# Kernel optimization log

Hardware: AMD Instinct MI355X
Metric: run time of the kernel (lower is better)

The kernel has to match this reference:

```python
import jax, jax.numpy as jnp
import numpy as np

NUM_NODES_G1 = 60000
NUM_NODES_G2 = 50000
NUM_REL = 16
NUM_BASES = 4
DIM = 128  # node_dim == hidden_dim == final_dim
L_COMMON = 100


def _concept_layer(x, edge_index):
    # Gather-based concept propagation: x_i <- x_i + mean_{j in N(i)} x_j
    src, dst = edge_index[0], edge_index[1]
    n = x.shape[0]
    agg = jax.ops.segment_sum(x[src], dst, num_segments=n)
    deg = jax.ops.segment_sum(jnp.ones((src.shape[0],), x.dtype), dst, num_segments=n)
    return x + agg / jnp.clip(deg, 1.0)[:, None]


def _rgcn_layer(x, edge_index, edge_type, basis, comp, root, bias):
    # Basis-decomposed RGCN: out_i = x_i @ root + bias + sum_r (1/|N_i^r|) sum_{j in N_i^r} x_j @ W_r,
    # W_r = sum_b comp[r,b] * basis[b]. Reorder: scatter comp-weighted x[src] per basis, then one GEMM per basis.
    src, dst = edge_index[0], edge_index[1]
    n = x.shape[0]
    e = src.shape[0]
    seg = dst * NUM_REL + edge_type  # per-(node, relation) bucket
    cnt = jax.ops.segment_sum(jnp.ones((e,), x.dtype), seg, num_segments=n * NUM_REL)
    norm = 1.0 / jnp.clip(cnt, 1.0)
    coef = comp[edge_type] * norm[seg][:, None]  # [E, B]
    xsrc = x[src]  # [E, D] -- dominant gather traffic
    out = x @ root + bias
    for b in range(NUM_BASES):  # small fixed loop over bases
        agg_b = jax.ops.segment_sum(xsrc * coef[:, b:b + 1], dst, num_segments=n)
        out = out + agg_b @ basis[b]
    return out


def setup_inputs() -> dict:
    key = jax.random.key(0)
    ks = jax.random.split(key, 16)
    e2, e1 = 800000, 800000
    return {
        "edge_index_g2": jax.random.randint(ks[0], (2, e2), 0, NUM_NODES_G2),
        "edge_type_g2": jax.random.randint(ks[1], (e2,), 0, NUM_REL),
        "edge_index_g1": jax.random.randint(ks[2], (2, e1), 0, NUM_NODES_G1),
        "left_common": jax.random.randint(ks[3], (L_COMMON,), 0, NUM_NODES_G1),
        "all_node_embedding": jax.random.normal(ks[4], (NUM_NODES_G1, DIM), jnp.float32),
        "basis1": jax.random.normal(ks[5], (NUM_BASES, DIM, DIM), jnp.float32) * 0.05,
        "comp1": jax.random.normal(ks[6], (NUM_REL, NUM_BASES), jnp.float32),
        "root1": jax.random.normal(ks[7], (DIM, DIM), jnp.float32) * 0.05,
        "bias1": jnp.zeros((DIM,), jnp.float32),
        "basis2": jax.random.normal(ks[8], (NUM_BASES, DIM, DIM), jnp.float32) * 0.05,
        "comp2": jax.random.normal(ks[9], (NUM_REL, NUM_BASES), jnp.float32),
        "root2": jax.random.normal(ks[10], (DIM, DIM), jnp.float32) * 0.05,
        "bias2": jnp.zeros((DIM,), jnp.float32),
        "weights": jax.random.uniform(ks[11], (DIM, 1), jnp.float32),
    }


def reference(edge_index_g2, edge_type_g2, edge_index_g1, left_common,
              all_node_embedding, basis1, comp1, root1, bias1,
              basis2, comp2, root2, bias2, weights):
    x_g1 = jax.nn.relu(_concept_layer(all_node_embedding, edge_index_g1))
    x = x_g1[:NUM_NODES_G2]
    x = _rgcn_layer(x, edge_index_g2, edge_type_g2, basis1, comp1, root1, bias1)
    x = jax.nn.relu(x)  # relu_use == 1
    x_g2 = _rgcn_layer(x, edge_index_g2, edge_type_g2, basis2, comp2, root2, bias2)
    ty = x_g1[left_common]  # [L, D]
    # mul_def outer elementwise product followed by matmul with weights collapses to one contraction:
    # logits[n,l] = sum_d x_g2[n,d] * ty[l,d] * w[d]
    logits = jnp.einsum('nd,ld,d->nl', x_g2, ty, weights[:, 0])
    return jax.nn.softmax(logits, axis=1)
```

## Files before the change

kernel.cpp:

```cpp
#include <hip/hip_runtime.h>
#include <hip/hip_bf16.h>
#include <math.h>

#define N1 60000
#define N2 50000
#define DIM 128
#define NREL 16
#define NB 4
#define LCOM 100
#define LPAD 112

typedef __attribute__((ext_vector_type(8))) short short8;
typedef __attribute__((ext_vector_type(4))) float f32x4;
typedef __attribute__((ext_vector_type(4))) _Float16 half4;
typedef __attribute__((ext_vector_type(8))) _Float16 half8;

__device__ __forceinline__ float bf2f(unsigned short u) {
    union { unsigned int i; float f; } c; c.i = ((unsigned int)u) << 16; return c.f;
}
__device__ __forceinline__ unsigned short f2bf(float f) {
    union { float f; unsigned int i; } c; c.f = f;
    unsigned int r = c.i + 0x7FFF + ((c.i >> 16) & 1);
    return (unsigned short)(r >> 16);
}
__device__ __forceinline__ void split8(float4 a, float4 b, short8& h, short8& l) {
    float f[8] = {a.x, a.y, a.z, a.w, b.x, b.y, b.z, b.w};
#pragma unroll
    for (int j = 0; j < 8; j++) {
        unsigned short hh = f2bf(f[j]);
        h[j] = (short)hh;
        l[j] = (short)f2bf(f[j] - bf2f(hh));
    }
}

__global__ __launch_bounds__(256) void k_prelude(
        const int* __restrict__ ei1, int E1, int* __restrict__ deg1, int HB1,
        const int* __restrict__ ei2, int E2, int* __restrict__ deg2, int HB2,
        const float* __restrict__ root1, const float* __restrict__ basis1,
        unsigned short* __restrict__ Wh1, unsigned short* __restrict__ Wl1,
        const float* __restrict__ root2, const float* __restrict__ basis2,
        unsigned short* __restrict__ Wh2, unsigned short* __restrict__ Wl2, int PB,
        const float* __restrict__ emb, _Float16* __restrict__ embh, int n4) {
    int b = blockIdx.x;
    if (b < HB1) {
        int e0 = b * 1024 + threadIdx.x;
#pragma unroll
        for (int j = 0; j < 4; j++) {
            int e = e0 + j * 256;
            if (e < E1) atomicAdd(deg1 + ei1[E1 + e], 1);
        }
    } else if (b < HB1 + HB2) {
        int e0 = (b - HB1) * 1024 + threadIdx.x;
#pragma unroll
        for (int j = 0; j < 4; j++) {
            int e = e0 + j * 256;
            if (e < E2) atomicAdd(deg2 + ei2[E2 + e], 1);
        }
    } else if (b < HB1 + HB2 + PB) {
        int t = (b - HB1 - HB2) * 256 + threadIdx.x;
        if (t < 2 * 640 * 128) {
            int which = t >= 640 * 128;
            int tt = which ? t - 640 * 128 : t;
            const float* root = which ? root2 : root1;
            const float* basis = which ? basis2 : basis1;
            unsigned short* Wh = which ? Wh2 : Wh1;
            unsigned short* Wl = which ? Wl2 : Wl1;
            int k = tt >> 7, n = tt & 127;
            float v = (k < 128) ? root[k * 128 + n] : basis[(k - 128) * 128 + n];
            unsigned short h = f2bf(v);
            Wh[n * 640 + k] = h;
            Wl[n * 640 + k] = f2bf(v - bf2f(h));
        }
    } else {
        int i = (b - HB1 - HB2 - PB) * 256 + threadIdx.x;
        if (i < n4) {
            float4 v = ((const float4*)emb)[i];
            half4 o = {(_Float16)v.x, (_Float16)v.y, (_Float16)v.z, (_Float16)v.w};
            ((half4*)embh)[i] = o;
        }
    }
}

__global__ __launch_bounds__(256) void k_scan_p1m(const int* __restrict__ inA, int nA, int nbA,
                                                  int* __restrict__ bsumA,
                                                  const int* __restrict__ inB, int nB,
                                                  int* __restrict__ bsumB) {
    __shared__ int red[256];
    const int* in; int n; int* bsum; int b;
    if ((int)blockIdx.x < nbA) { in = inA; n = nA; bsum = bsumA; b = blockIdx.x; }
    else { in = inB; n = nB; bsum = bsumB; b = blockIdx.x - nbA; }
    int base = b * 1024;
    int tid = threadIdx.x;
    int s = 0;
#pragma unroll
    for (int j = 0; j < 4; j++) {
        int i = base + tid * 4 + j;
        if (i < n) s += in[i];
    }
    red[tid] = s;
    __syncthreads();
    for (int d = 128; d; d >>= 1) {
        if (tid < d) red[tid] += red[tid + d];
        __syncthreads();
    }
    if (tid == 0) bsum[b] = red[0];
}

__global__ __launch_bounds__(64) void k_scan_p2m(const int* __restrict__ bsumA, int* __restrict__ boffA,
                                                 int* __restrict__ offA, int nbA, int nA,
                                                 const int* __restrict__ bsumB, int* __restrict__ boffB,
                                                 int* __restrict__ offB, int nbB, int nB) {
    __shared__ int s[64];
    const int* bsum; int* boff; int* off; int nb; int n;
    if (blockIdx.x == 0) { bsum = bsumA; boff = boffA; off = offA; nb = nbA; n = nA; }
    else { bsum = bsumB; boff = boffB; off = offB; nb = nbB; n = nB; }
    int tid = threadIdx.x;
    int v = (tid < nb) ? bsum[tid] : 0;
    s[tid] = v;
    __syncthreads();
    for (int d = 1; d < 64; d <<= 1) {
        int t = (tid >= d) ? s[tid - d] : 0;
        __syncthreads();
        s[tid] += t;
        __syncthreads();
    }
    if (tid < nb) boff[tid] = s[tid] - v;
    if (tid == 63) off[n] = s[63];
}

__global__ __launch_bounds__(256) void k_scan_p3m(const int* __restrict__ inA, const int* __restrict__ boffA,
                                                  int* __restrict__ offA, int* __restrict__ curA,
                                                  int nA, int nbA,
                                                  const int* __restrict__ inB, const int* __restrict__ boffB,
                                                  int* __restrict__ offB, int* __restrict__ curB, int nB) {
    __shared__ int red[256];
    const int* in; const int* boff; int* off; int* cur; int n; int b;
    if ((int)blockIdx.x < nbA) { in = inA; boff = boffA; off = offA; cur = curA; n = nA; b = blockIdx.x; }
    else { in = inB; boff = boffB; off = offB; cur = curB; n = nB; b = blockIdx.x - nbA; }
    int base = b * 1024;
    int tid = threadIdx.x;
    int v[4];
    int s = 0;
#pragma unroll
    for (int j = 0; j < 4; j++) {
        int i = base + tid * 4 + j;
        v[j] = (i < n) ? in[i] : 0;
        s += v[j];
    }
    red[tid] = s;
    __syncthreads();
    for (int d = 1; d < 256; d <<= 1) {
        int t = (tid >= d) ? red[tid - d] : 0;
        __syncthreads();
        red[tid] += t;
        __syncthreads();
    }
    int run = boff[b] + red[tid] - s;
#pragma unroll
    for (int j = 0; j < 4; j++) {
        int i = base + tid * 4 + j;
        if (i < n) {
            off[i] = run; cur[i] = run;
            run += v[j];
        }
    }
}

__global__ __launch_bounds__(256) void k_scat(const int* __restrict__ ei1, int E1,
                                              int* __restrict__ cur1, int* __restrict__ elist1, int HB1,
                                              const int* __restrict__ ei2, const int* __restrict__ et2,
                                              int E2, int* __restrict__ cur2, int* __restrict__ elist2) {
    int b = blockIdx.x;
    if (b < HB1) {
        int e0 = b * 1024 + threadIdx.x;
#pragma unroll
        for (int j = 0; j < 4; j++) {
            int e = e0 + j * 256;
            if (e < E1) {
                int pos = atomicAdd(cur1 + ei1[E1 + e], 1);
                elist1[pos] = ei1[e];
            }
        }
    } else {
        int e0 = (b - HB1) * 1024 + threadIdx.x;
#pragma unroll
        for (int j = 0; j < 4; j++) {
            int e = e0 + j * 256;
            if (e < E2) {
                int pos = atomicAdd(cur2 + ei2[E2 + e], 1);
                elist2[pos] = (ei2[e] << 4) | et2[e];
            }
        }
    }
}

__global__ __launch_bounds__(256) void k_mix(
        const _Float16* __restrict__ embh, const float* __restrict__ emb,
        const int* __restrict__ off1, const int* __restrict__ elist1,
        float* __restrict__ xg1, _Float16* __restrict__ xg1h, int CONC_B,
        const int* __restrict__ lc, const float* __restrict__ w,
        unsigned short* __restrict__ tyh, unsigned short* __restrict__ tyl) {
    int b = blockIdx.x;
    if (b < CONC_B) {
        int node = b * 4 + (threadIdx.x >> 6);
        int lane = threadIdx.x & 63;
        if (node >= N2) return;
        int quad = lane >> 4, d8 = (lane & 15) * 8;
        int s0 = off1[node], s1 = off1[node + 1];
        float acc[8] = {};
        int i = s0;
        for (; i + 8 <= s1; i += 8) {
            int sa = elist1[i + quad];
            int sb = elist1[i + 4 + quad];
            half8 ha = *(const half8*)(embh + (size_t)sa * DIM + d8);
            half8 hb = *(const half8*)(embh + (size_t)sb * DIM + d8);
#pragma unroll
            for (int j = 0; j < 8; j++) acc[j] += (float)ha[j] + (float)hb[j];
        }
        if (i + 4 <= s1) {
            int sa = elist1[i + quad];
            half8 ha = *(const half8*)(embh + (size_t)sa * DIM + d8);
#pragma unroll
            for (int j = 0; j < 8; j++) acc[j] += (float)ha[j];
            i += 4;
        }
        if (i < s1) {
            int e = i + quad;
            bool ok = e < s1;
            int s = elist1[ok ? e : i];
            half8 hv = *(const half8*)(embh + (size_t)s * DIM + d8);
            if (ok) {
#pragma unroll
                for (int j = 0; j < 8; j++) acc[j] += (float)hv[j];
            }
        }
#pragma unroll
        for (int j = 0; j < 8; j++) {
            acc[j] += __shfl_xor(acc[j], 16, 64);
            acc[j] += __shfl_xor(acc[j], 32, 64);
        }
        if (quad == 0) {
            float inv = 1.0f / (float)max(s1 - s0, 1);
            const float* ep = emb + (size_t)node * DIM + d8;
            float4 e0 = *(const float4*)(ep);
            float4 e1 = *(const float4*)(ep + 4);
            float o[8];
            o[0] = fmaxf(e0.x + acc[0] * inv, 0.f);
            o[1] = fmaxf(e0.y + acc[1] * inv, 0.f);
            o[2] = fmaxf(e0.z + acc[2] * inv, 0.f);
            o[3] = fmaxf(e0.w + acc[3] * inv, 0.f);
            o[4] = fmaxf(e1.x + acc[4] * inv, 0.f);
            o[5] = fmaxf(e1.y + acc[5] * inv, 0.f);
            o[6] = fmaxf(e1.z + acc[6] * inv, 0.f);
            o[7] = fmaxf(e1.w + acc[7] * inv, 0.f);
            float4 w0 = {o[0], o[1], o[2], o[3]};
            float4 w1 = {o[4], o[5], o[6], o[7]};
            *(float4*)(xg1 + (size_t)node * DIM + d8) = w0;
            *(float4*)(xg1 + (size_t)node * DIM + d8 + 4) = w1;
            half8 oh;
#pragma unroll
            for (int j = 0; j < 8; j++) oh[j] = (_Float16)o[j];
            *(half8*)(xg1h + (size_t)node * DIM + d8) = oh;
        }
    } else {
        if (threadIdx.x >= 64) return;
        int l = b - CONC_B;
        int lane = threadIdx.x;
        int d0 = lane * 2;
        if (l >= LCOM) {
            ushort2 z = {0, 0};
            *(ushort2*)(tyh + (size_t)l * 128 + d0) = z;
            *(ushort2*)(tyl + (size_t)l * 128 + d0) = z;
            return;
        }
        int row = lc[l];
        int s0 = off1[row], s1 = off1[row + 1];
        float2 acc = {0.f, 0.f};
        for (int i = s0; i < s1; i++) {
            int s = elist1[i];
            float2 v = *(const float2*)(emb + (size_t)s * DIM + lane * 2);
            acc.x += v.x; acc.y += v.y;
        }
        float inv = 1.0f / (float)max(s1 - s0, 1);
        float2 e = *(const float2*)(emb + (size_t)row * DIM + lane * 2);
        float v0 = fmaxf(e.x + acc.x * inv, 0.f) * w[d0];
        float v1 = fmaxf(e.y + acc.y * inv, 0.f) * w[d0 + 1];
        unsigned short h0 = f2bf(v0), h1 = f2bf(v1);
        ushort2 hh = {h0, h1};
        ushort2 ll = {f2bf(v0 - bf2f(h0)), f2bf(v1 - bf2f(h1))};
        *(ushort2*)(tyh + (size_t)l * 128 + d0) = hh;
        *(ushort2*)(tyl + (size_t)l * 128 + d0) = ll;
    }
}

__global__ __launch_bounds__(256) void k_rgcn_gather(const _Float16* __restrict__ xh,
                                                     const int* __restrict__ off,
                                                     const int* __restrict__ elist,
                                                     const float* __restrict__ comp,
                                                     float* __restrict__ agg, int n) {
    __shared__ float scomp[NREL * NB];
    __shared__ float nrmlds[4][NREL];
    if (threadIdx.x < NREL * NB) scomp[threadIdx.x] = comp[threadIdx.x];
    __syncthreads();
    int nb = threadIdx.x >> 6;
    int node = blockIdx.x * 4 + nb;
    int lane = threadIdx.x & 63;
    if (node >= n) return;
    int s0 = off[node], s1 = off[node + 1];
    unsigned long long c0 = 0, c1 = 0;
    for (int i = s0 + lane; i < s1; i += 64) {
        int t = elist[i] & 15;
        if (t < 8) c0 += 1ull << (8 * t); else c1 += 1ull << (8 * (t - 8));
    }
#pragma unroll
    for (int o = 32; o; o >>= 1) {
        c0 += __shfl_xor(c0, o, 64);
        c1 += __shfl_xor(c1, o, 64);
    }
    if (lane < NREL) {
        unsigned int c = (lane < 8) ? (unsigned int)((c0 >> (8 * lane)) & 255)
                                    : (unsigned int)((c1 >> (8 * (lane - 8))) & 255);
        nrmlds[nb][lane] = 1.0f / (float)max(c, 1u);
    }
    int quad = lane >> 4, d8 = (lane & 15) * 8;
    float a[4][8] = {};
#define RGE(P, GATE)                                                           \
    {                                                                          \
        int s_ = (P) >> 4, t_ = (P) & 15;                                      \
        float nr_ = nrmlds[nb][t_] * (GATE);                                   \
        float4 cf_ = *(const float4*)(scomp + t_ * 4);                         \
        half8 hv_ = *(const half8*)(xh + (size_t)s_ * DIM + d8);               \
        float c0_ = cf_.x * nr_, c1_ = cf_.y * nr_;                            \
        float c2_ = cf_.z * nr_, c3_ = cf_.w * nr_;                            \
        _Pragma("unroll")                                                      \
        for (int j = 0; j < 8; j++) {                                          \
            float v_ = (float)hv_[j];                                          \
            a[0][j] = fmaf(c0_, v_, a[0][j]);                                  \
            a[1][j] = fmaf(c1_, v_, a[1][j]);                                  \
            a[2][j] = fmaf(c2_, v_, a[2][j]);                                  \
            a[3][j] = fmaf(c3_, v_, a[3][j]);                                  \
        }                                                                      \
    }
    int i = s0;
    for (; i + 8 <= s1; i += 8) {
        int pa = elist[i + quad];
        int pb = elist[i + 4 + quad];
        RGE(pa, 1.0f);
        RGE(pb, 1.0f);
    }
    if (i + 4 <= s1) {
        int pa = elist[i + quad];
        RGE(pa, 1.0f);
        i += 4;
    }
    if (i < s1) {
        int e = i + quad;
        bool ok = e < s1;
        int pa = elist[ok ? e : i];
        RGE(pa, ok ? 1.0f : 0.0f);
    }
#undef RGE
#pragma unroll
    for (int bb = 0; bb < 4; bb++)
#pragma unroll
        for (int j = 0; j < 8; j++) {
            a[bb][j] += __shfl_xor(a[bb][j], 16, 64);
            a[bb][j] += __shfl_xor(a[bb][j], 32, 64);
        }
    if (quad == 0) {
        float* o = agg + (size_t)node * (NB * DIM) + d8;
#pragma unroll
        for (int bb = 0; bb < 4; bb++) {
            float4 v0 = {a[bb][0], a[bb][1], a[bb][2], a[bb][3]};
            float4 v1 = {a[bb][4], a[bb][5], a[bb][6], a[bb][7]};
            *(float4*)(o + bb * DIM) = v0;
            *(float4*)(o + bb * DIM + 4) = v1;
        }
    }
}

#define LDSK 40
__global__ __launch_bounds__(256) void k_gemm(const float* __restrict__ x,
                                              const float* __restrict__ agg,
                                              const unsigned short* __restrict__ Wh,
                                              const unsigned short* __restrict__ Wl,
                                              const float* __restrict__ bias,
                                              float* __restrict__ out,
                                              _Float16* __restrict__ out_h, int relu) {
    __shared__ __align__(16) short Ah[128 * LDSK];
    __shared__ __align__(16) short Al[128 * LDSK];
    __shared__ __align__(16) short Bh[128 * LDSK];
    __shared__ __align__(16) short Bl[128 * LDSK];
    int tid = threadIdx.x;
    int lane = tid & 63, wid = tid >> 6;
    int wave_m = wid >> 1, wave_n = wid & 1;
    int l15 = lane & 15, quad = lane >> 4;
    int row0 = blockIdx.x * 128;

    int srow = tid >> 1, skh = (tid & 1) * 16;

    f32x4 acc[4][4] = {};
    for (int k0 = 0; k0 < 640; k0 += 32) {
        {
            int rg = row0 + srow;
            float4 q0 = {0, 0, 0, 0}, q1 = q0, q2 = q0, q3 = q0;
            if (rg < N2) {
                const float* src = (k0 < 128) ? (x + (size_t)rg * 128 + k0 + skh)
                                              : (agg + (size_t)rg * 512 + (k0 - 128) + skh);
                q0 = *(const float4*)(src + 0);
                q1 = *(const float4*)(src + 4);
                q2 = *(const float4*)(src + 8);
                q3 = *(const float4*)(src + 12);
            }
            short8 h0, l0, h1, l1;
            split8(q0, q1, h0, l0);
            split8(q2, q3, h1, l1);
            *(short8*)(&Ah[srow * LDSK + skh]) = h0;
            *(short8*)(&Ah[srow * LDSK + skh + 8]) = h1;
            *(short8*)(&Al[srow * LDSK + skh]) = l0;
            *(short8*)(&Al[srow * LDSK + skh + 8]) = l1;
        }
        {
            const unsigned short* sh = Wh + (size_t)srow * 640 + k0 + skh;
            const unsigned short* sl = Wl + (size_t)srow * 640 + k0 + skh;
            *(short8*)(&Bh[srow * LDSK + skh]) = *(const short8*)(sh);
            *(short8*)(&Bh[srow * LDSK + skh + 8]) = *(const short8*)(sh + 8);
            *(short8*)(&Bl[srow * LDSK + skh]) = *(const short8*)(sl);
            *(short8*)(&Bl[srow * LDSK + skh + 8]) = *(const short8*)(sl + 8);
        }
        __syncthreads();
        short8 ah[4], al[4], bh[4], bl[4];
#pragma unroll
        for (int i = 0; i < 4; i++) {
            int ro = (wave_m * 64 + i * 16 + l15) * LDSK + quad * 8;
            ah[i] = *(const short8*)(&Ah[ro]);
            al[i] = *(const short8*)(&Al[ro]);
        }
#pragma unroll
        for (int j = 0; j < 4; j++) {
            int ro = (wave_n * 64 + j * 16 + l15) * LDSK + quad * 8;
            bh[j] = *(const short8*)(&Bh[ro]);
            bl[j] = *(const short8*)(&Bl[ro]);
        }
#pragma unroll
        for (int i = 0; i < 4; i++)
#pragma unroll
            for (int j = 0; j < 4; j++) {
                acc[i][j] = __builtin_amdgcn_mfma_f32_16x16x32_bf16(al[i], bh[j], acc[i][j], 0, 0, 0);
                acc[i][j] = __builtin_amdgcn_mfma_f32_16x16x32_bf16(ah[i], bl[j], acc[i][j], 0, 0, 0);
                acc[i][j] = __builtin_amdgcn_mfma_f32_16x16x32_bf16(ah[i], bh[j], acc[i][j], 0, 0, 0);
            }
        __syncthreads();
    }
#pragma unroll
    for (int j = 0; j < 4; j++) {
        int gcol = wave_n * 64 + j * 16 + l15;
        float bv = bias[gcol];
#pragma unroll
        for (int i = 0; i < 4; i++) {
            int grow_base = row0 + wave_m * 64 + i * 16 + quad * 4;
#pragma unroll
            for (int r = 0; r < 4; r++) {
                int grow = grow_base + r;
                if (grow >= N2) continue;
                float v = acc[i][j][r] + bv;
                if (relu) v = fmaxf(v, 0.f);
                out[(size_t)grow * 128 + gcol] = v;
                if (out_h) out_h[(size_t)grow * 128 + gcol] = (_Float16)v;
            }
        }
    }
}

__global__ __launch_bounds__(256) void k_logits(const float* __restrict__ h2,
                                                const unsigned short* __restrict__ tyh,
                                                const unsigned short* __restrict__ tyl,
                                                float* __restrict__ out, int M) {
    int wid = threadIdx.x >> 6, lane = threadIdx.x & 63;
    int l15 = lane & 15, quad = lane >> 4;
    int row0w = blockIdx.x * 64 + wid * 16;
    int arow = min(row0w + l15, M - 1);
    f32x4 acc[7] = {};
#pragma unroll
    for (int k0 = 0; k0 < 128; k0 += 32) {
        const float* ap = h2 + (size_t)arow * 128 + k0 + quad * 8;
        float4 q0 = *(const float4*)(ap);
        float4 q1 = *(const float4*)(ap + 4);
        short8 ah, al;
        split8(q0, q1, ah, al);
#pragma unroll
        for (int j = 0; j < 7; j++) {
            size_t bo = (size_t)(j * 16 + l15) * 128 + k0 + quad * 8;
            short8 bh = *(const short8*)(tyh + bo);
            short8 bl = *(const short8*)(tyl + bo);
            acc[j] = __builtin_amdgcn_mfma_f32_16x16x32_bf16(al, bh, acc[j], 0, 0, 0);
            acc[j] = __builtin_amdgcn_mfma_f32_16x16x32_bf16(ah, bl, acc[j], 0, 0, 0);
            acc[j] = __builtin_amdgcn_mfma_f32_16x16x32_bf16(ah, bh, acc[j], 0, 0, 0);
        }
    }
    bool v6 = (l15 < LCOM - 96);
#pragma unroll
    for (int r = 0; r < 4; r++) {
        int grow = row0w + quad * 4 + r;
        float m = -INFINITY;
#pragma unroll
        for (int j = 0; j < 6; j++) m = fmaxf(m, acc[j][r]);
        if (v6) m = fmaxf(m, acc[6][r]);
        m = fmaxf(m, __shfl_xor(m, 8, 64));
        m = fmaxf(m, __shfl_xor(m, 4, 64));
        m = fmaxf(m, __shfl_xor(m, 2, 64));
        m = fmaxf(m, __shfl_xor(m, 1, 64));
        float e[7];
        float s = 0.f;
#pragma unroll
        for (int j = 0; j < 6; j++) { e[j] = __expf(acc[j][r] - m); s += e[j]; }
        e[6] = v6 ? __expf(acc[6][r] - m) : 0.f;
        s += e[6];
        s += __shfl_xor(s, 8, 64);
        s += __shfl_xor(s, 4, 64);
        s += __shfl_xor(s, 2, 64);
        s += __shfl_xor(s, 1, 64);
        float inv = 1.0f / s;
        if (grow < M) {
#pragma unroll
            for (int j = 0; j < 6; j++) out[(size_t)grow * LCOM + j * 16 + l15] = e[j] * inv;
            if (v6) out[(size_t)grow * LCOM + 96 + l15] = e[6] * inv;
        }
    }
}

extern "C" void kernel_launch(void* const* d_in, const int* in_sizes, int n_in,
                              void* d_out, int out_size, void* d_ws, size_t ws_size,
                              hipStream_t stream) {
    const int* ei2 = (const int*)d_in[0];
    const int* et2 = (const int*)d_in[1];
    const int* ei1 = (const int*)d_in[2];
    const int* lc = (const int*)d_in[3];
    const float* emb = (const float*)d_in[4];
    const float* basis1 = (const float*)d_in[5];
    const float* comp1 = (const float*)d_in[6];
    const float* root1 = (const float*)d_in[7];
    const float* bias1 = (const float*)d_in[8];
    const float* basis2 = (const float*)d_in[9];
    const float* comp2 = (const float*)d_in[10];
    const float* root2 = (const float*)d_in[11];
    const float* bias2 = (const float*)d_in[12];
    const float* wts = (const float*)d_in[13];
    float* out = (float*)d_out;
    int E2 = in_sizes[0] / 2, E1 = in_sizes[2] / 2;

    float* ws = (float*)d_ws;
    float* xg1 = ws;
    float* h1 = xg1 + 6400000;
    float* agg = h1 + 6400000;
    _Float16* emb_h = (_Float16*)(agg + 25600000);
    unsigned short* tyh = (unsigned short*)(emb_h + 7680000);
    unsigned short* tyl = tyh + LPAD * 128;
    unsigned short* Wh1 = tyl + LPAD * 128;
    unsigned short* Wl1 = Wh1 + 81920;
    unsigned short* Wh2 = Wl1 + 81920;
    unsigned short* Wl2 = Wh2 + 81920;
    int* ipool = (int*)(Wl2 + 81920);
    int* deg1 = ipool;
    int* deg2 = deg1 + 60000;
    int* off1 = deg2 + 50000;
    int* cur1 = off1 + 60001;
    int* elist1 = cur1 + 60000;
    int* off2 = elist1 + 800000;
    int* cur2 = off2 + 50001;
    int* elist2 = cur2 + 50000;
    int* bsum1 = elist2 + 800000;
    int* boff1 = bsum1 + 64;
    int* bsum2 = boff1 + 64;
    int* boff2 = bsum2 + 64;
    _Float16* xg1_h = (_Float16*)h1;
    _Float16* h1_h = emb_h;
    float* h2 = xg1;

    const int NB1 = (N1 + 1023) / 1024;
    const int NB2 = (N2 + 1023) / 1024;
    const int HB1 = (E1 + 1023) / 1024;
    const int HB2 = (E2 + 1023) / 1024;
    const int PB = (2 * 640 * 128) / 256;
    const int CB = (N1 * DIM / 4 + 255) / 256;
    const int CONC_B = (N2 + 3) / 4;

    hipMemsetAsync(deg1, 0, (60000 + 50000) * sizeof(int), stream);

    k_prelude<<<HB1 + HB2 + PB + CB, 256, 0, stream>>>(
        ei1, E1, deg1, HB1, ei2, E2, deg2, HB2,
        root1, basis1, Wh1, Wl1, root2, basis2, Wh2, Wl2, PB,
        emb, emb_h, N1 * DIM / 4);

    k_scan_p1m<<<NB1 + NB2, 256, 0, stream>>>(deg1, N1, NB1, bsum1, deg2, N2, bsum2);
    k_scan_p2m<<<2, 64, 0, stream>>>(bsum1, boff1, off1, NB1, N1, bsum2, boff2, off2, NB2, N2);
    k_scan_p3m<<<NB1 + NB2, 256, 0, stream>>>(deg1, boff1, off1, cur1, N1, NB1,
                                              deg2, boff2, off2, cur2, N2);

    k_scat<<<HB1 + HB2, 256, 0, stream>>>(ei1, E1, cur1, elist1, HB1,
                                          ei2, et2, E2, cur2, elist2);

    k_mix<<<CONC_B + LPAD, 256, 0, stream>>>(
        emb_h, emb, off1, elist1, xg1, xg1_h, CONC_B,
        lc, wts, tyh, tyl);

    k_rgcn_gather<<<CONC_B, 256, 0, stream>>>(xg1_h, off2, elist2, comp1, agg, N2);
    k_gemm<<<(N2 + 127) / 128, 256, 0, stream>>>(xg1, agg, Wh1, Wl1, bias1, h1, h1_h, 1);

    k_rgcn_gather<<<CONC_B, 256, 0, stream>>>(h1_h, off2, elist2, comp2, agg, N2);
    k_gemm<<<(N2 + 127) / 128, 256, 0, stream>>>(h1, agg, Wh2, Wl2, bias2, h2, (_Float16*)nullptr, 0);

    k_logits<<<(N2 + 63) / 64, 256, 0, stream>>>(h2, tyh, tyl, out, N2);
}
```

Before: 591.9 us.

## Partition edge scatter by destination range to localize atomics and writes

The CSR scatter kernel now launches 8 partitions per edge chunk. Each block reads a contiguous chunk of edges and handles only those whose destination falls in its partition's node range. This is meant to keep the atomic counters and the element-list writes for each block within a smaller address window, improving cache locality. In exchange, the destination array is read 8 times, blocks do redundant filtering, and the grid becomes a fixed 2048 blocks that each loop over a larger chunk.

```diff
diff --git a/kernel.cpp b/kernel.cpp
--- a/kernel.cpp
+++ b/kernel.cpp
@@ -9,6 +9,7 @@
 #define NB 4
 #define LCOM 100
 #define LPAD 112
+#define NPART 8
 
 typedef __attribute__((ext_vector_type(8))) short short8;
 typedef __attribute__((ext_vector_type(4))) float f32x4;
@@ -167,28 +168,57 @@
 }
 
 __global__ __launch_bounds__(256) void k_scat(const int* __restrict__ ei1, int E1,
-                                              int* __restrict__ cur1, int* __restrict__ elist1, int HB1,
+                                              int* __restrict__ cur1, int* __restrict__ elist1, int G1,
                                               const int* __restrict__ ei2, const int* __restrict__ et2,
-                                              int E2, int* __restrict__ cur2, int* __restrict__ elist2) {
-    int b = blockIdx.x;
-    if (b < HB1) {
-        int e0 = b * 1024 + threadIdx.x;
-#pragma unroll
-        for (int j = 0; j < 4; j++) {
-            int e = e0 + j * 256;
-            if (e < E1) {
-                int pos = atomicAdd(cur1 + ei1[E1 + e], 1);
-                elist1[pos] = ei1[e];
+                                              int E2, int* __restrict__ cur2, int* __restrict__ elist2,
+                                              int G2) {
+    int p = blockIdx.x & (NPART - 1);
+    int c = blockIdx.x >> 3;
+    if (c < G1) {
+        const int W = (N1 + NPART - 1) / NPART;
+        int lo = p * W, hi = min(lo + W, N1);
+        int chunk = (E1 + G1 - 1) / G1;
+        int e0 = c * chunk, e1 = min(e0 + chunk, E1);
+        for (int base = e0; base < e1; base += 1024) {
+            int d[4]; bool ok[4];
+#pragma unroll
+            for (int j = 0; j < 4; j++) {
+                int e = base + threadIdx.x + j * 256;
+                bool inb = e < e1;
+                d[j] = inb ? ei1[E1 + e] : -1;
+                ok[j] = inb && d[j] >= lo && d[j] < hi;
+            }
+#pragma unroll
+            for (int j = 0; j < 4; j++) {
+                if (ok[j]) {
+                    int e = base + threadIdx.x + j * 256;
+                    int pos = atomicAdd(cur1 + d[j], 1);
+                    elist1[pos] = ei1[e];
+                }
             }
         }
     } else {
-        int e0 = (b - HB1) * 1024 + threadIdx.x;
-#pragma unroll
-        for (int j = 0; j < 4; j++) {
-            int e = e0 + j * 256;
-            if (e < E2) {
-                int pos = atomicAdd(cur2 + ei2[E2 + e], 1);
-                elist2[pos] = (ei2[e] << 4) | et2[e];
+        c -= G1;
+        const int W = (N2 + NPART - 1) / NPART;
+        int lo = p * W, hi = min(lo + W, N2);
+        int chunk = (E2 + G2 - 1) / G2;
+        int e0 = c * chunk, e1 = min(e0 + chunk, E2);
+        for (int base = e0; base < e1; base += 1024) {
+            int d[4]; bool ok[4];
+#pragma unroll
+            for (int j = 0; j < 4; j++) {
+                int e = base + threadIdx.x + j * 256;
+                bool inb = e < e1;
+                d[j] = inb ? ei2[E2 + e] : -1;
+                ok[j] = inb && d[j] >= lo && d[j] < hi;
+            }
+#pragma unroll
+            for (int j = 0; j < 4; j++) {
+                if (ok[j]) {
+                    int e = base + threadIdx.x + j * 256;
+                    int pos = atomicAdd(cur2 + d[j], 1);
+                    elist2[pos] = (ei2[e] << 4) | et2[e];
+                }
             }
         }
     }
@@ -584,6 +614,7 @@
     const int PB = (2 * 640 * 128) / 256;
     const int CB = (N1 * DIM / 4 + 255) / 256;
     const int CONC_B = (N2 + 3) / 4;
+    const int G1 = 128, G2 = 128;
 
     hipMemsetAsync(deg1, 0, (60000 + 50000) * sizeof(int), stream);
 
@@ -597,8 +628,8 @@
     k_scan_p3m<<<NB1 + NB2, 256, 0, stream>>>(deg1, boff1, off1, cur1, N1, NB1,
                                               deg2, boff2, off2, cur2, N2);
 
-    k_scat<<<HB1 + HB2, 256, 0, stream>>>(ei1, E1, cur1, elist1, HB1,
-                                          ei2, et2, E2, cur2, elist2);
+    k_scat<<<NPART * (G1 + G2), 256, 0, stream>>>(ei1, E1, cur1, elist1, G1,
+                                                  ei2, et2, E2, cur2, elist2, G2);
 
     k_mix<<<CONC_B + LPAD, 256, 0, stream>>>(
         emb_h, emb, off1, elist1, xg1, xg1_h, CONC_B,
```

After: 559.5 us. 5.5% less time.

## Replace atomic CSR scatter with two-pass bucketed binning and LDS placement

Applied to the files above, without the earlier changes.

The single-pass scatter, which did one global atomic per edge on the per-node cursor, becomes a two-pass build. The first pass bins edges by coarse destination bucket through an LDS staging area, doing one global atomic per bucket flush. The second pass places each bucket's edges with LDS atomics into a shared-memory window and writes them out coalesced. Edge-index loads also switch to nontemporal loads. The change aims to cut global atomic contention and scattered writes, at the cost of an extra kernel and extra traffic through a temporary pair buffer that aliases the agg buffer.

```diff
diff --git a/kernel.cpp b/kernel.cpp
--- a/kernel.cpp
+++ b/kernel.cpp
@@ -9,6 +9,15 @@
 #define NB 4
 #define LCOM 100
 #define LPAD 112
+
+#define NBUK1 59
+#define NBUK2 98
+#define BIN_G 128
+#define BATCH 4096
+#define CAP1 128
+#define CAP2 80
+#define STAGE_SZ 7936
+#define WCAP 16384
 
 typedef __attribute__((ext_vector_type(8))) short short8;
 typedef __attribute__((ext_vector_type(4))) float f32x4;
@@ -47,14 +56,14 @@
 #pragma unroll
         for (int j = 0; j < 4; j++) {
             int e = e0 + j * 256;
-            if (e < E1) atomicAdd(deg1 + ei1[E1 + e], 1);
+            if (e < E1) atomicAdd(deg1 + __builtin_nontemporal_load(ei1 + E1 + e), 1);
         }
     } else if (b < HB1 + HB2) {
         int e0 = (b - HB1) * 1024 + threadIdx.x;
 #pragma unroll
         for (int j = 0; j < 4; j++) {
             int e = e0 + j * 256;
-            if (e < E2) atomicAdd(deg2 + ei2[E2 + e], 1);
+            if (e < E2) atomicAdd(deg2 + __builtin_nontemporal_load(ei2 + E2 + e), 1);
         }
     } else if (b < HB1 + HB2 + PB) {
         int t = (b - HB1 - HB2) * 256 + threadIdx.x;
@@ -130,13 +139,14 @@
 
 __global__ __launch_bounds__(256) void k_scan_p3m(const int* __restrict__ inA, const int* __restrict__ boffA,
                                                   int* __restrict__ offA, int* __restrict__ curA,
-                                                  int nA, int nbA,
+                                                  int nA, int nbA, int* __restrict__ bcurA,
                                                   const int* __restrict__ inB, const int* __restrict__ boffB,
-                                                  int* __restrict__ offB, int* __restrict__ curB, int nB) {
+                                                  int* __restrict__ offB, int* __restrict__ curB, int nB,
+                                                  int* __restrict__ bcurB) {
     __shared__ int red[256];
-    const int* in; const int* boff; int* off; int* cur; int n; int b;
-    if ((int)blockIdx.x < nbA) { in = inA; boff = boffA; off = offA; cur = curA; n = nA; b = blockIdx.x; }
-    else { in = inB; boff = boffB; off = offB; cur = curB; n = nB; b = blockIdx.x - nbA; }
+    const int* in; const int* boff; int* off; int* cur; int n; int b; int* bcur; int bsh;
+    if ((int)blockIdx.x < nbA) { in = inA; boff = boffA; off = offA; cur = curA; n = nA; b = blockIdx.x; bcur = bcurA; bsh = 10; }
+    else { in = inB; boff = boffB; off = offB; cur = curB; n = nB; b = blockIdx.x - nbA; bcur = bcurB; bsh = 9; }
     int base = b * 1024;
     int tid = threadIdx.x;
     int v[4];
@@ -156,40 +166,102 @@
         __syncthreads();
     }
     int run = boff[b] + red[tid] - s;
+    int msk = (1 << bsh) - 1;
 #pragma unroll
     for (int j = 0; j < 4; j++) {
         int i = base + tid * 4 + j;
         if (i < n) {
             off[i] = run; cur[i] = run;
+            if ((i & msk) == 0) bcur[i >> bsh] = run;
             run += v[j];
         }
     }
 }
 
-__global__ __launch_bounds__(256) void k_scat(const int* __restrict__ ei1, int E1,
-                                              int* __restrict__ cur1, int* __restrict__ elist1, int HB1,
-                                              const int* __restrict__ ei2, const int* __restrict__ et2,
-                                              int E2, int* __restrict__ cur2, int* __restrict__ elist2) {
+__global__ __launch_bounds__(256) void k_bin(
+        const int* __restrict__ ei1, int E1, int* __restrict__ bcur1, int2* __restrict__ binbuf1,
+        const int* __restrict__ ei2, const int* __restrict__ et2, int E2,
+        int* __restrict__ bcur2, int2* __restrict__ binbuf2) {
+    __shared__ int scnt[128];
+    __shared__ int2 stage[STAGE_SZ];
+    int isg2 = blockIdx.x >= BIN_G;
+    int c = blockIdx.x & (BIN_G - 1);
+    const int* ei = isg2 ? ei2 : ei1;
+    int E = isg2 ? E2 : E1;
+    int* bcur = isg2 ? bcur2 : bcur1;
+    int2* binbuf = isg2 ? binbuf2 : binbuf1;
+    int shift = isg2 ? 9 : 10;
+    int CAP = isg2 ? CAP2 : CAP1;
+    int nbuk = isg2 ? NBUK2 : NBUK1;
+    int chunk = (E + BIN_G - 1) / BIN_G;
+    int e0 = c * chunk, e1 = min(e0 + chunk, E);
+    int tid = threadIdx.x;
+    int wid = tid >> 6, lane = tid & 63;
+    for (int base = e0; base < e1; base += BATCH) {
+        for (int i = tid; i < nbuk; i += 256) scnt[i] = 0;
+        __syncthreads();
+#pragma unroll
+        for (int j = 0; j < 16; j++) {
+            int e = base + tid + j * 256;
+            if (e < e1) {
+                int d = __builtin_nontemporal_load(ei + E + e);
+                int s = __builtin_nontemporal_load(ei + e);
+                int pay = isg2 ? ((s << 4) | __builtin_nontemporal_load(et2 + e)) : s;
+                int b = d >> shift;
+                int pos = atomicAdd(&scnt[b], 1);
+                int2 pr; pr.x = d; pr.y = pay;
+                if (pos < CAP) {
+                    stage[b * CAP + pos] = pr;
+                } else {
+                    int g = atomicAdd(&bcur[b], 1);
+                    binbuf[g] = pr;
+                }
+            }
+        }
+        __syncthreads();
+        for (int b = wid; b < nbuk; b += 4) {
+            int cc = min(scnt[b], CAP);
+            if (cc > 0) {
+                int gbase = 0;
+                if (lane == 0) gbase = atomicAdd(&bcur[b], cc);
+                gbase = __shfl(gbase, 0, 64);
+                for (int k = lane; k < cc; k += 64) binbuf[gbase + k] = stage[b * CAP + k];
+            }
+        }
+        __syncthreads();
+    }
+}
+
+__global__ __launch_bounds__(256) void k_place(
+        const int* __restrict__ off1, int* __restrict__ cur1,
+        const int2* __restrict__ binbuf1, int* __restrict__ elist1,
+        const int* __restrict__ off2, int* __restrict__ cur2,
+        const int2* __restrict__ binbuf2, int* __restrict__ elist2) {
+    __shared__ int win[WCAP];
+    __shared__ int lcur[1024];
     int b = blockIdx.x;
-    if (b < HB1) {
-        int e0 = b * 1024 + threadIdx.x;
-#pragma unroll
-        for (int j = 0; j < 4; j++) {
-            int e = e0 + j * 256;
-            if (e < E1) {
-                int pos = atomicAdd(cur1 + ei1[E1 + e], 1);
-                elist1[pos] = ei1[e];
-            }
-        }
+    const int* off; int* cur; const int2* binbuf; int* elist; int lo, W, N;
+    if (b < NBUK1) { off = off1; cur = cur1; binbuf = binbuf1; elist = elist1; lo = b << 10; W = 1024; N = N1; }
+    else { b -= NBUK1; off = off2; cur = cur2; binbuf = binbuf2; elist = elist2; lo = b << 9; W = 512; N = N2; }
+    int hi = min(lo + W, N);
+    int tid = threadIdx.x;
+    int base = off[lo];
+    int cnt = off[hi] - base;
+    for (int i = tid; i < hi - lo; i += 256) lcur[i] = off[lo + i] - base;
+    __syncthreads();
+    if (cnt <= WCAP) {
+        for (int k = tid; k < cnt; k += 256) {
+            int2 pr = binbuf[base + k];
+            int pos = atomicAdd(&lcur[pr.x - lo], 1);
+            win[pos] = pr.y;
+        }
+        __syncthreads();
+        for (int k = tid; k < cnt; k += 256) elist[base + k] = win[k];
     } else {
-        int e0 = (b - HB1) * 1024 + threadIdx.x;
-#pragma unroll
-        for (int j = 0; j < 4; j++) {
-            int e = e0 + j * 256;
-            if (e < E2) {
-                int pos = atomicAdd(cur2 + ei2[E2 + e], 1);
-                elist2[pos] = (ei2[e] << 4) | et2[e];
-            }
+        for (int k = tid; k < cnt; k += 256) {
+            int2 pr = binbuf[base + k];
+            int pos = atomicAdd(&cur[pr.x], 1);
+            elist[pos] = pr.y;
         }
     }
 }
@@ -573,6 +645,10 @@
     int* boff1 = bsum1 + 64;
     int* bsum2 = boff1 + 64;
     int* boff2 = bsum2 + 64;
+    int* bcur1 = boff2 + 64;
+    int* bcur2 = bcur1 + 64;
+    int2* binbuf1 = (int2*)agg;
+    int2* binbuf2 = binbuf1 + 800000;
     _Float16* xg1_h = (_Float16*)h1;
     _Float16* h1_h = emb_h;
     float* h2 = xg1;
@@ -594,11 +670,14 @@
 
     k_scan_p1m<<<NB1 + NB2, 256, 0, stream>>>(deg1, N1, NB1, bsum1, deg2, N2, bsum2);
     k_scan_p2m<<<2, 64, 0, stream>>>(bsum1, boff1, off1, NB1, N1, bsum2, boff2, off2, NB2, N2);
-    k_scan_p3m<<<NB1 + NB2, 256, 0, stream>>>(deg1, boff1, off1, cur1, N1, NB1,
-                                              deg2, boff2, off2, cur2, N2);
-
-    k_scat<<<HB1 + HB2, 256, 0, stream>>>(ei1, E1, cur1, elist1, HB1,
-                                          ei2, et2, E2, cur2, elist2);
+    k_scan_p3m<<<NB1 + NB2, 256, 0, stream>>>(deg1, boff1, off1, cur1, N1, NB1, bcur1,
+                                              deg2, boff2, off2, cur2, N2, bcur2);
+
+    k_bin<<<2 * BIN_G, 256, 0, stream>>>(ei1, E1, bcur1, binbuf1,
+                                         ei2, et2, E2, bcur2, binbuf2);
+
+    k_place<<<NBUK1 + NBUK2, 256, 0, stream>>>(off1, cur1, binbuf1, elist1,
+                                               off2, cur2, binbuf2, elist2);
 
     k_mix<<<CONC_B + LPAD, 256, 0, stream>>>(
         emb_h, emb, off1, elist1, xg1, xg1_h, CONC_B,
```

Result: slower. 626.6 us (+5.9%).
